# Kernel optimization log

Measured on AMD Instinct MI355X. Metric: run time of the kernel, lower is better.

Reference implementation:

```python
import jax, jax.numpy as jnp
import numpy as np

H, KV, D = 16, 4, 128
WIN = 512
EPS = 1e-6


def rms_norm(x, w):
    # x: [..., D]
    return x * jax.lax.rsqrt(jnp.mean(x * x, axis=-1, keepdims=True) + EPS) * w


def rotate_half(x):
    x1, x2 = jnp.split(x, 2, axis=-1)
    return jnp.concatenate([-x2, x1], axis=-1)


def setup_inputs() -> dict:
    key = jax.random.key(0)
    ks = jax.random.split(key, 8)
    B, L, hidden = 2, 2048, 2048
    x = jax.random.normal(ks[0], (B, L, hidden), jnp.float32)
    # realistic RoPE tables
    inv_freq = 1.0 / (10000.0 ** (np.arange(0, D, 2, dtype=np.float32) / D))
    t = np.arange(L, dtype=np.float32)
    freqs = np.outer(t, inv_freq)  # [L, D/2]
    emb = np.concatenate([freqs, freqs], axis=-1)  # [L, D]
    cos = jnp.asarray(np.cos(emb), jnp.float32)
    sin = jnp.asarray(np.sin(emb), jnp.float32)
    s = 0.02
    Wq = jax.random.normal(ks[1], (H * D, hidden), jnp.float32) * s
    Wk = jax.random.normal(ks[2], (KV * D, hidden), jnp.float32) * s
    Wv = jax.random.normal(ks[3], (KV * D, hidden), jnp.float32) * s
    Wo = jax.random.normal(ks[4], (hidden, H * D), jnp.float32) * s
    q_norm_w = jnp.ones((D,), jnp.float32)
    k_norm_w = jnp.ones((D,), jnp.float32)
    return {"x": x, "cos": cos, "sin": sin, "Wq": Wq, "Wk": Wk, "Wv": Wv,
            "Wo": Wo, "q_norm_w": q_norm_w, "k_norm_w": k_norm_w}


def reference(x, cos, sin, Wq, Wk, Wv, Wo, q_norm_w, k_norm_w):
    B, L, _ = x.shape
    # projections (torch Linear: y = x @ W.T)
    q = (x @ Wq.T).reshape(B, L, H, D)
    k = (x @ Wk.T).reshape(B, L, KV, D)
    v = (x @ Wv.T).reshape(B, L, KV, D)
    # QK RMSNorm, then [B, heads, L, D]
    q = jnp.transpose(rms_norm(q, q_norm_w), (0, 2, 1, 3))
    k = jnp.transpose(rms_norm(k, k_norm_w), (0, 2, 1, 3))
    v = jnp.transpose(v, (0, 2, 1, 3))
    # RoPE
    c = cos[None, None]  # [1,1,L,D]
    s = sin[None, None]
    q = q * c + rotate_half(q) * s
    k = k * c + rotate_half(k) * s
    # GQA repeat_interleave over head dim
    n_rep = H // KV
    k = jnp.repeat(k, n_rep, axis=1)
    v = jnp.repeat(v, n_rep, axis=1)
    # sliding-window additive bias [L, L]
    idx = jnp.arange(L)
    in_win = jnp.abs(idx[:, None] - idx[None, :]) <= WIN
    bias = jnp.where(in_win, 0.0, jnp.finfo(x.dtype).min).astype(x.dtype)
    # SDPA
    scale = 1.0 / jnp.sqrt(jnp.asarray(D, x.dtype))
    scores = jnp.einsum('bhqd,bhkd->bhqk', q, k) * scale + bias[None, None]
    attn = jax.nn.softmax(scores, axis=-1)
    out = jnp.einsum('bhqk,bhkd->bhqd', attn, v)  # [B,H,L,D]
    out = jnp.transpose(out, (0, 2, 1, 3)).reshape(B, L, H * D)
    return out @ Wo.T
```

## Files before the change

### kernel.cpp

```cpp
#include <hip/hip_runtime.h>
#include <hip/hip_bf16.h>


typedef unsigned short u16;
typedef unsigned int u32;
typedef __attribute__((ext_vector_type(8))) short bf16x8;
typedef __attribute__((ext_vector_type(4))) float f32x4;

#define AS1 __attribute__((address_space(1)))
#define AS3 __attribute__((address_space(3)))

__device__ __forceinline__ u16 f2b(float f) {
  union { float f; u32 u; } c; c.f = f;
  return (u16)((c.u + 0x8000u) >> 16);
}
__device__ __forceinline__ float b2f(u16 u) {
  union { u32 u; float f; } c; c.u = ((u32)u) << 16; return c.f;
}

__global__ __launch_bounds__(256) void cvt_all(const float* __restrict__ x,
                                               const float* __restrict__ wq,
                                               const float* __restrict__ wk,
                                               const float* __restrict__ wv,
                                               const float* __restrict__ wo,
                                               u16* __restrict__ xb,
                                               u16* __restrict__ wqkvb,
                                               u16* __restrict__ wob) {
  int blk = blockIdx.x;
  const float* s; u16* d; int off;
  if (blk < 8192)       { s = x;  d = xb;              off = blk * 1024; }
  else if (blk < 12288) { s = wq; d = wqkvb;           off = (blk - 8192) * 1024; }
  else if (blk < 13312) { s = wk; d = wqkvb + 4194304; off = (blk - 12288) * 1024; }
  else if (blk < 14336) { s = wv; d = wqkvb + 5242880; off = (blk - 13312) * 1024; }
  else                  { s = wo; d = wob;             off = (blk - 14336) * 1024; }
  int i = off + threadIdx.x * 4;
  float4 v = *(const float4*)(s + i);
  ushort4 o;
  o.x = f2b(v.x); o.y = f2b(v.y); o.z = f2b(v.z); o.w = f2b(v.w);
  *(ushort4*)(d + i) = o;
}

template<int F32OUT>
__global__ __launch_bounds__(256) void gemm_bt(const u16* __restrict__ A,
                                               const u16* __restrict__ Bm,
                                               void* __restrict__ C,
                                               int M, int N, int K) {
  __shared__ u16 As[128][64];
  __shared__ u16 Bs[128][64];
  const int tid  = threadIdx.x;
  const int w    = tid >> 6, lane = tid & 63, quad = lane >> 4, l16 = lane & 15;
  const int wm   = w >> 1, wn = w & 1;
  const int m0   = blockIdx.y * 128, n0 = blockIdx.x * 128;

  f32x4 zero = {0.f, 0.f, 0.f, 0.f};
  f32x4 acc[4][4];
#pragma unroll
  for (int i = 0; i < 4; i++)
#pragma unroll
    for (int j = 0; j < 4; j++) acc[i][j] = zero;

  const int srow = lane >> 3;
  const int swz8 = ((lane & 7) ^ (lane >> 3)) * 8;

  for (int k0 = 0; k0 < K; k0 += 64) {
#pragma unroll
    for (int p = 0; p < 4; ++p) {
      int row = p * 32 + w * 8 + srow;
      __builtin_amdgcn_global_load_lds(
          (const AS1 void*)(A + (size_t)(m0 + row) * K + k0 + swz8),
          (AS3 void*)((char*)&As[0][0] + p * 4096 + w * 1024), 16, 0, 0);
      __builtin_amdgcn_global_load_lds(
          (const AS1 void*)(Bm + (size_t)(n0 + row) * K + k0 + swz8),
          (AS3 void*)((char*)&Bs[0][0] + p * 4096 + w * 1024), 16, 0, 0);
    }
    __syncthreads();
#pragma unroll
    for (int kk = 0; kk < 64; kk += 32) {
      const int cs = ((kk >> 3) + quad) ^ (l16 & 7);
      bf16x8 af[4], bfr[4];
#pragma unroll
      for (int i = 0; i < 4; i++)
        af[i] = *(const bf16x8*)((const char*)&As[0][0] +
                                 (wm * 64 + i * 16 + l16) * 128 + cs * 16);
#pragma unroll
      for (int j = 0; j < 4; j++)
        bfr[j] = *(const bf16x8*)((const char*)&Bs[0][0] +
                                  (wn * 64 + j * 16 + l16) * 128 + cs * 16);
#pragma unroll
      for (int i = 0; i < 4; i++)
#pragma unroll
        for (int j = 0; j < 4; j++)
          acc[i][j] = __builtin_amdgcn_mfma_f32_16x16x32_bf16(af[i], bfr[j], acc[i][j], 0, 0, 0);
    }
    __syncthreads();
  }

#pragma unroll
  for (int i = 0; i < 4; i++) {
#pragma unroll
    for (int r = 0; r < 4; r++) {
      int gr = m0 + wm * 64 + i * 16 + quad * 4 + r;
#pragma unroll
      for (int j = 0; j < 4; j++) {
        int gc = n0 + wn * 64 + j * 16 + l16;
        if (F32OUT) ((float*)C)[(size_t)gr * N + gc] = acc[i][j][r];
        else        ((u16*)C)[(size_t)gr * N + gc]   = f2b(acc[i][j][r]);
      }
    }
  }
}

__global__ __launch_bounds__(256) void rmsrope(const u16* __restrict__ qkv,
                                               const float* __restrict__ cosT,
                                               const float* __restrict__ sinT,
                                               const float* __restrict__ qw,
                                               const float* __restrict__ kw,
                                               u16* __restrict__ qo,
                                               u16* __restrict__ ko) {
  int wid  = blockIdx.x * 4 + (threadIdx.x >> 6);
  int lane = threadIdx.x & 63;
  int r  = wid / 20;
  int hh = wid % 20;
  int b = r >> 11, l = r & 2047;
  int cb = hh < 16 ? hh * 128 : 2048 + (hh - 16) * 128;
  const u16* src = qkv + (size_t)r * 3072 + cb;
  float v0 = b2f(src[lane]);
  float v1 = b2f(src[lane + 64]);
  float ss = v0 * v0 + v1 * v1;
#pragma unroll
  for (int off = 1; off < 64; off <<= 1) ss += __shfl_xor(ss, off, 64);
  float inv = rsqrtf(ss * (1.0f / 128.0f) + 1e-6f);
  const float* wt = hh < 16 ? qw : kw;
  float n0 = v0 * inv * wt[lane];
  float n1 = v1 * inv * wt[lane + 64];
  float c0 = cosT[l * 128 + lane],      c1 = cosT[l * 128 + 64 + lane];
  float s0 = sinT[l * 128 + lane],      s1 = sinT[l * 128 + 64 + lane];
  float o0 = n0 * c0 - n1 * s0;
  float o1 = n1 * c1 + n0 * s1;
  const float qscale = 0.08838834764831845f * 1.4426950408889634f;
  u16* dst; size_t base;
  if (hh < 16) { dst = qo; base = ((size_t)(b * 16 + hh) * 2048 + l) * 128;
                 o0 *= qscale; o1 *= qscale; }
  else         { dst = ko; base = ((size_t)(b * 4 + (hh - 16)) * 2048 + l) * 128; }
  dst[base + lane]      = f2b(o0);
  dst[base + 64 + lane] = f2b(o1);
}

__global__ __launch_bounds__(256) void transpose_v(const u16* __restrict__ qkv,
                                                   u16* __restrict__ dst) {
  __shared__ u16 T[64][72];
  const int lt = blockIdx.x, dt = blockIdx.y, bh = blockIdx.z;
  const int b = bh >> 2, kv = bh & 3;
  const u16* s = qkv + ((size_t)(b * 2048 + lt * 64)) * 3072 + 2560 + kv * 128 + dt * 64;
  u16*       d = dst + (size_t)bh * 128 * 2048 + (size_t)dt * 64 * 2048 + lt * 64;
  const int t = threadIdx.x;
  const int row = t >> 3, c8 = (t & 7) * 8;
#pragma unroll
  for (int p = 0; p < 2; ++p)
    *(uint4*)&T[p * 32 + row][c8] = *(const uint4*)(s + (size_t)(p * 32 + row) * 3072 + c8);
  __syncthreads();
#pragma unroll
  for (int p = 0; p < 2; ++p) {
    int dr = p * 32 + row;
    u16 o[8];
#pragma unroll
    for (int j = 0; j < 8; ++j) o[j] = T[c8 + j][dr];
    *(uint4*)(d + (size_t)dr * 2048 + c8) = *(uint4*)o;
  }
}

__global__ __launch_bounds__(256) void flash_swa(const u16* __restrict__ Q,
                                                 const u16* __restrict__ Kg,
                                                 const u16* __restrict__ VTg,
                                                 u16* __restrict__ Og) {
  constexpr int L = 2048, D = 128;
  __shared__ u16 Ks[2][64][128];
  __shared__ u16 Vt[2][128][64];
  __shared__ u16 Ps[4][16][64];

  const int q0  = blockIdx.x * 64;
  const int h   = blockIdx.y;
  const int b   = blockIdx.z;
  const int tid = threadIdx.x;
  const int w = tid >> 6, lane = tid & 63, quad = lane >> 4, l16 = lane & 15;
  const int kvh = h >> 2;

  const u16* Qb  = Q   + (size_t)(b * 16 + h)  * L * D;
  const u16* Kb  = Kg  + (size_t)(b * 4 + kvh) * L * D;
  const u16* VTb = VTg + (size_t)(b * 4 + kvh) * D * L;

  bf16x8 qf[4];
  {
    int qr = q0 + w * 16 + l16;
#pragma unroll
    for (int ks = 0; ks < 4; ++ks)
      qf[ks] = *(const bf16x8*)(Qb + (size_t)qr * D + ks * 32 + quad * 8);
  }
  const int qi = q0 + w * 16 + l16;

  int kt0   = q0 > 512 ? q0 - 512 : 0;
  int ktend = q0 + 64 + 512; if (ktend > L) ktend = L;
  const int nt = (ktend - kt0) >> 6;

  const u16* srcK[4];
  const u16* srcV[4];
#pragma unroll
  for (int p = 0; p < 4; ++p) {
    int rk = w * 16 + p * 4 + (lane >> 4);
    int ck = ((lane & 15) ^ (rk & 7)) * 8;
    srcK[p] = Kb + (size_t)(kt0 + rk) * D + ck;
    int rv = w * 32 + p * 8 + (lane >> 3);
    int cv = ((lane & 7) ^ (rv & 7)) * 8;
    srcV[p] = VTb + (size_t)rv * L + kt0 + cv;
  }

#define STAGE(bb) do {                                                        \
    char* kdst = (char*)&Ks[bb][0][0] + w * 4096;                             \
    char* vdst = (char*)&Vt[bb][0][0] + w * 4096;                             \
    _Pragma("unroll")                                                         \
    for (int p = 0; p < 4; ++p) {                                             \
      __builtin_amdgcn_global_load_lds((const AS1 void*)srcK[p],              \
          (AS3 void*)(kdst + p * 1024), 16, 0, 0);                            \
      srcK[p] += 64 * D;                                                      \
    }                                                                         \
    _Pragma("unroll")                                                         \
    for (int p = 0; p < 4; ++p) {                                             \
      __builtin_amdgcn_global_load_lds((const AS1 void*)srcV[p],              \
          (AS3 void*)(vdst + p * 1024), 16, 0, 0);                            \
      srcV[p] += 64;                                                          \
    }                                                                         \
  } while (0)

  f32x4 zero = {0.f, 0.f, 0.f, 0.f};
  f32x4 o[8];
#pragma unroll
  for (int i = 0; i < 8; i++) o[i] = zero;
  float lrow = 0.f;

  STAGE(0);
  __syncthreads();
  int cur = 0;

  const int swz = (l16 & 7) << 4;

  for (int t = 0; t < nt; ++t) {
    const int kt = kt0 + t * 64;
    if (t + 1 < nt) STAGE(cur ^ 1);

    const char* kbase = (const char*)&Ks[cur][0][0];
    const char* vbase = (const char*)&Vt[cur][0][0];

    f32x4 s[4];
#pragma unroll
    for (int ct = 0; ct < 4; ct++) s[ct] = zero;
    __builtin_amdgcn_s_setprio(1);
#pragma unroll
    for (int ks = 0; ks < 4; ++ks) {
#pragma unroll
      for (int ct = 0; ct < 4; ++ct) {
        bf16x8 kf = *(const bf16x8*)(kbase + (ct * 16 + l16) * 256 +
                                     (((ks * 4 + quad) ^ (l16 & 7)) * 16));
        s[ct] = __builtin_amdgcn_mfma_f32_16x16x32_bf16(kf, qf[ks], s[ct], 0, 0, 0);
      }
    }
    __builtin_amdgcn_s_setprio(0);

    bool need_mask = (kt + 448 < q0) || (kt > q0 + 448);
    float psum = 0.f;
    char* psw = (char*)&Ps[w][l16][0];
#pragma unroll
    for (int ct = 0; ct < 4; ct++) {
      u16 ph[4];
#pragma unroll
      for (int r = 0; r < 4; r++) {
        float x = s[ct][r];
        if (need_mask) {
          int ki = kt + ct * 16 + quad * 4 + r;
          int dd = qi - ki; if (dd < 0) dd = -dd;
          if (dd > 512) x = -__builtin_inff();
        }
        float p = exp2f(x);
        psum += p;
        ph[r] = f2b(p);
      }
      uint2 pk;
      pk.x = (u32)ph[0] | ((u32)ph[1] << 16);
      pk.y = (u32)ph[2] | ((u32)ph[3] << 16);
      *(uint2*)(psw + ((ct * 32 + quad * 8) ^ swz)) = pk;
    }
    psum += __shfl_xor(psum, 16, 64);
    psum += __shfl_xor(psum, 32, 64);
    lrow += psum;

    bf16x8 pf[2];
#pragma unroll
    for (int ks2 = 0; ks2 < 2; ++ks2)
      pf[ks2] = *(const bf16x8*)(psw + ((ks2 * 64 + quad * 16) ^ swz));
    __builtin_amdgcn_s_setprio(1);
#pragma unroll
    for (int dt = 0; dt < 8; ++dt) {
#pragma unroll
      for (int ks2 = 0; ks2 < 2; ++ks2) {
        bf16x8 vf = *(const bf16x8*)(vbase + (dt * 16 + l16) * 128 +
                                     (((ks2 * 4 + quad) ^ (l16 & 7)) * 16));
        o[dt] = __builtin_amdgcn_mfma_f32_16x16x32_bf16(pf[ks2], vf, o[dt], 0, 0, 0);
      }
    }
    __builtin_amdgcn_s_setprio(0);

    __syncthreads();
    cur ^= 1;
  }
#undef STAGE

#pragma unroll
  for (int r = 0; r < 4; r++) {
    float lv  = __shfl(lrow, (lane & 48) + quad * 4 + r, 64);
    float inv = 1.0f / lv;
    int qr = q0 + w * 16 + quad * 4 + r;
    size_t base = ((size_t)(b * L + qr)) * 2048 + h * 128;
#pragma unroll
    for (int dt = 0; dt < 8; dt++)
      Og[base + dt * 16 + l16] = f2b(o[dt][r] * inv);
  }
}

extern "C" void kernel_launch(void* const* d_in, const int* in_sizes, int n_in,
                              void* d_out, int out_size, void* d_ws, size_t ws_size,
                              hipStream_t stream) {
  const float* x    = (const float*)d_in[0];
  const float* cosT = (const float*)d_in[1];
  const float* sinT = (const float*)d_in[2];
  const float* Wq   = (const float*)d_in[3];
  const float* Wk   = (const float*)d_in[4];
  const float* Wv   = (const float*)d_in[5];
  const float* Wo   = (const float*)d_in[6];
  const float* qw   = (const float*)d_in[7];
  const float* kw   = (const float*)d_in[8];

  char* ws = (char*)d_ws;
  u16* x_bf    = (u16*)(ws + 0);
  u16* wqkv_bf = (u16*)(ws + 16777216);
  u16* wo_bf   = (u16*)(ws + 29360128);
  u16* qkv_bf  = (u16*)(ws + 37748736);
  u16* q_bf    = (u16*)(ws + 62914560);
  u16* k_bf    = (u16*)(ws + 79691776);
  u16* vt_bf   = wqkv_bf;
  u16* attn_bf = x_bf;

  cvt_all<<<18432, 256, 0, stream>>>(x, Wq, Wk, Wv, Wo, x_bf, wqkv_bf, wo_bf);
  gemm_bt<0><<<dim3(24, 32), 256, 0, stream>>>(x_bf, wqkv_bf, qkv_bf, 4096, 3072, 2048);
  rmsrope<<<20480, 256, 0, stream>>>(qkv_bf, cosT, sinT, qw, kw, q_bf, k_bf);
  transpose_v<<<dim3(32, 2, 8), 256, 0, stream>>>(qkv_bf, vt_bf);
  flash_swa<<<dim3(32, 16, 2), 256, 0, stream>>>(q_bf, k_bf, vt_bf, attn_bf);
  gemm_bt<1><<<dim3(16, 32), 256, 0, stream>>>(attn_bf, wo_bf, d_out, 4096, 2048, 2048);
}
```

Baseline: 315.4 us.

## Share K/V tiles across all four GQA heads in one 512-thread flash block

Each attention block now handles all four query heads that share one KV head, with 8 waves each covering 32 query rows of one head, so every K/V tile staged into LDS is reused by four heads instead of being reloaded per head. The grid shrinks from 1024 to 256 blocks of 512 threads, and each wave keeps two 16-row Q fragments and two sets of accumulators. This cuts global K/V traffic, at the cost of higher register pressure, a larger P scratch buffer, and fewer blocks, which may leave CUs underused.

Measured after the change: 299.8 us. 1.05x faster.

```diff
diff --git a/kernel.cpp b/kernel.cpp
--- a/kernel.cpp
+++ b/kernel.cpp
@@ -169,73 +169,77 @@
   }
 }
 
-__global__ __launch_bounds__(256) void flash_swa(const u16* __restrict__ Q,
+__global__ __launch_bounds__(512) void flash_swa(const u16* __restrict__ Q,
                                                  const u16* __restrict__ Kg,
                                                  const u16* __restrict__ VTg,
                                                  u16* __restrict__ Og) {
   constexpr int L = 2048, D = 128;
   __shared__ u16 Ks[2][64][128];
   __shared__ u16 Vt[2][128][64];
-  __shared__ u16 Ps[4][16][64];
+  __shared__ u16 Ps[8][32][64];
 
   const int q0  = blockIdx.x * 64;
-  const int h   = blockIdx.y;
+  const int kvh = blockIdx.y;
   const int b   = blockIdx.z;
   const int tid = threadIdx.x;
   const int w = tid >> 6, lane = tid & 63, quad = lane >> 4, l16 = lane & 15;
-  const int kvh = h >> 2;
-
-  const u16* Qb  = Q   + (size_t)(b * 16 + h)  * L * D;
+  const int hd = kvh * 4 + (w >> 1);
+  const int qh = w & 1;
+
+  const u16* Qb  = Q   + (size_t)(b * 16 + hd)  * L * D;
   const u16* Kb  = Kg  + (size_t)(b * 4 + kvh) * L * D;
   const u16* VTb = VTg + (size_t)(b * 4 + kvh) * D * L;
 
-  bf16x8 qf[4];
-  {
-    int qr = q0 + w * 16 + l16;
+  bf16x8 qf[2][4];
+#pragma unroll
+  for (int qs = 0; qs < 2; ++qs) {
+    int qr = q0 + qh * 32 + qs * 16 + l16;
 #pragma unroll
     for (int ks = 0; ks < 4; ++ks)
-      qf[ks] = *(const bf16x8*)(Qb + (size_t)qr * D + ks * 32 + quad * 8);
-  }
-  const int qi = q0 + w * 16 + l16;
+      qf[qs][ks] = *(const bf16x8*)(Qb + (size_t)qr * D + ks * 32 + quad * 8);
+  }
+  const int qi0 = q0 + qh * 32 + l16;
 
   int kt0   = q0 > 512 ? q0 - 512 : 0;
   int ktend = q0 + 64 + 512; if (ktend > L) ktend = L;
   const int nt = (ktend - kt0) >> 6;
 
-  const u16* srcK[4];
-  const u16* srcV[4];
-#pragma unroll
-  for (int p = 0; p < 4; ++p) {
-    int rk = w * 16 + p * 4 + (lane >> 4);
+  const u16* srcK[2];
+  const u16* srcV[2];
+#pragma unroll
+  for (int j = 0; j < 2; ++j) {
+    int rk = w * 8 + j * 4 + quad;
     int ck = ((lane & 15) ^ (rk & 7)) * 8;
-    srcK[p] = Kb + (size_t)(kt0 + rk) * D + ck;
-    int rv = w * 32 + p * 8 + (lane >> 3);
-    int cv = ((lane & 7) ^ (rv & 7)) * 8;
-    srcV[p] = VTb + (size_t)rv * L + kt0 + cv;
+    srcK[j] = Kb + (size_t)(kt0 + rk) * D + ck;
+    int rv = w * 16 + j * 8 + (lane >> 3);
+    int cv = ((lane & 7) ^ ((lane >> 3) & 7)) * 8;
+    srcV[j] = VTb + (size_t)rv * L + kt0 + cv;
   }
 
 #define STAGE(bb) do {                                                        \
-    char* kdst = (char*)&Ks[bb][0][0] + w * 4096;                             \
-    char* vdst = (char*)&Vt[bb][0][0] + w * 4096;                             \
+    char* kdst = (char*)&Ks[bb][0][0] + w * 2048;                             \
+    char* vdst = (char*)&Vt[bb][0][0] + w * 2048;                             \
     _Pragma("unroll")                                                         \
-    for (int p = 0; p < 4; ++p) {                                             \
-      __builtin_amdgcn_global_load_lds((const AS1 void*)srcK[p],              \
-          (AS3 void*)(kdst + p * 1024), 16, 0, 0);                            \
-      srcK[p] += 64 * D;                                                      \
+    for (int j = 0; j < 2; ++j) {                                             \
+      __builtin_amdgcn_global_load_lds((const AS1 void*)srcK[j],              \
+          (AS3 void*)(kdst + j * 1024), 16, 0, 0);                            \
+      srcK[j] += 64 * D;                                                      \
     }                                                                         \
     _Pragma("unroll")                                                         \
-    for (int p = 0; p < 4; ++p) {                                             \
-      __builtin_amdgcn_global_load_lds((const AS1 void*)srcV[p],              \
-          (AS3 void*)(vdst + p * 1024), 16, 0, 0);                            \
-      srcV[p] += 64;                                                          \
+    for (int j = 0; j < 2; ++j) {                                             \
+      __builtin_amdgcn_global_load_lds((const AS1 void*)srcV[j],              \
+          (AS3 void*)(vdst + j * 1024), 16, 0, 0);                            \
+      srcV[j] += 64;                                                          \
     }                                                                         \
   } while (0)
 
   f32x4 zero = {0.f, 0.f, 0.f, 0.f};
-  f32x4 o[8];
-#pragma unroll
-  for (int i = 0; i < 8; i++) o[i] = zero;
-  float lrow = 0.f;
+  f32x4 o[2][8];
+#pragma unroll
+  for (int qs = 0; qs < 2; ++qs)
+#pragma unroll
+    for (int i = 0; i < 8; i++) o[qs][i] = zero;
+  float lrow[2] = {0.f, 0.f};
 
   STAGE(0);
   __syncthreads();
@@ -250,9 +254,11 @@
     const char* kbase = (const char*)&Ks[cur][0][0];
     const char* vbase = (const char*)&Vt[cur][0][0];
 
-    f32x4 s[4];
-#pragma unroll
-    for (int ct = 0; ct < 4; ct++) s[ct] = zero;
+    f32x4 s[2][4];
+#pragma unroll
+    for (int qs = 0; qs < 2; ++qs)
+#pragma unroll
+      for (int ct = 0; ct < 4; ct++) s[qs][ct] = zero;
     __builtin_amdgcn_s_setprio(1);
 #pragma unroll
     for (int ks = 0; ks < 4; ++ks) {
@@ -260,42 +266,50 @@
       for (int ct = 0; ct < 4; ++ct) {
         bf16x8 kf = *(const bf16x8*)(kbase + (ct * 16 + l16) * 256 +
                                      (((ks * 4 + quad) ^ (l16 & 7)) * 16));
-        s[ct] = __builtin_amdgcn_mfma_f32_16x16x32_bf16(kf, qf[ks], s[ct], 0, 0, 0);
+        s[0][ct] = __builtin_amdgcn_mfma_f32_16x16x32_bf16(kf, qf[0][ks], s[0][ct], 0, 0, 0);
+        s[1][ct] = __builtin_amdgcn_mfma_f32_16x16x32_bf16(kf, qf[1][ks], s[1][ct], 0, 0, 0);
       }
     }
     __builtin_amdgcn_s_setprio(0);
 
     bool need_mask = (kt + 448 < q0) || (kt > q0 + 448);
-    float psum = 0.f;
-    char* psw = (char*)&Ps[w][l16][0];
-#pragma unroll
-    for (int ct = 0; ct < 4; ct++) {
-      u16 ph[4];
-#pragma unroll
-      for (int r = 0; r < 4; r++) {
-        float x = s[ct][r];
-        if (need_mask) {
-          int ki = kt + ct * 16 + quad * 4 + r;
-          int dd = qi - ki; if (dd < 0) dd = -dd;
-          if (dd > 512) x = -__builtin_inff();
+#pragma unroll
+    for (int qs = 0; qs < 2; ++qs) {
+      float psum = 0.f;
+      char* psw = (char*)&Ps[w][qs * 16 + l16][0];
+#pragma unroll
+      for (int ct = 0; ct < 4; ct++) {
+        u16 ph[4];
+#pragma unroll
+        for (int r = 0; r < 4; r++) {
+          float x = s[qs][ct][r];
+          if (need_mask) {
+            int ki = kt + ct * 16 + quad * 4 + r;
+            int dd = (qi0 + qs * 16) - ki; if (dd < 0) dd = -dd;
+            if (dd > 512) x = -__builtin_inff();
+          }
+          float p = exp2f(x);
+          psum += p;
+          ph[r] = f2b(p);
         }
-        float p = exp2f(x);
-        psum += p;
-        ph[r] = f2b(p);
+        uint2 pk;
+        pk.x = (u32)ph[0] | ((u32)ph[1] << 16);
+        pk.y = (u32)ph[2] | ((u32)ph[3] << 16);
+        *(uint2*)(psw + ((ct * 32 + quad * 8) ^ swz)) = pk;
       }
-      uint2 pk;
-      pk.x = (u32)ph[0] | ((u32)ph[1] << 16);
-      pk.y = (u32)ph[2] | ((u32)ph[3] << 16);
-      *(uint2*)(psw + ((ct * 32 + quad * 8) ^ swz)) = pk;
-    }
-    psum += __shfl_xor(psum, 16, 64);
-    psum += __shfl_xor(psum, 32, 64);
-    lrow += psum;
-
-    bf16x8 pf[2];
-#pragma unroll
-    for (int ks2 = 0; ks2 < 2; ++ks2)
-      pf[ks2] = *(const bf16x8*)(psw + ((ks2 * 64 + quad * 16) ^ swz));
+      psum += __shfl_xor(psum, 16, 64);
+      psum += __shfl_xor(psum, 32, 64);
+      lrow[qs] += psum;
+    }
+
+    bf16x8 pf[2][2];
+#pragma unroll
+    for (int qs = 0; qs < 2; ++qs) {
+      const char* psw = (const char*)&Ps[w][qs * 16 + l16][0];
+#pragma unroll
+      for (int ks2 = 0; ks2 < 2; ++ks2)
+        pf[qs][ks2] = *(const bf16x8*)(psw + ((ks2 * 64 + quad * 16) ^ swz));
+    }
     __builtin_amdgcn_s_setprio(1);
 #pragma unroll
     for (int dt = 0; dt < 8; ++dt) {
@@ -303,7 +317,8 @@
       for (int ks2 = 0; ks2 < 2; ++ks2) {
         bf16x8 vf = *(const bf16x8*)(vbase + (dt * 16 + l16) * 128 +
                                      (((ks2 * 4 + quad) ^ (l16 & 7)) * 16));
-        o[dt] = __builtin_amdgcn_mfma_f32_16x16x32_bf16(pf[ks2], vf, o[dt], 0, 0, 0);
+        o[0][dt] = __builtin_amdgcn_mfma_f32_16x16x32_bf16(pf[0][ks2], vf, o[0][dt], 0, 0, 0);
+        o[1][dt] = __builtin_amdgcn_mfma_f32_16x16x32_bf16(pf[1][ks2], vf, o[1][dt], 0, 0, 0);
       }
     }
     __builtin_amdgcn_s_setprio(0);
@@ -314,14 +329,17 @@
 #undef STAGE
 
 #pragma unroll
-  for (int r = 0; r < 4; r++) {
-    float lv  = __shfl(lrow, (lane & 48) + quad * 4 + r, 64);
-    float inv = 1.0f / lv;
-    int qr = q0 + w * 16 + quad * 4 + r;
-    size_t base = ((size_t)(b * L + qr)) * 2048 + h * 128;
-#pragma unroll
-    for (int dt = 0; dt < 8; dt++)
-      Og[base + dt * 16 + l16] = f2b(o[dt][r] * inv);
+  for (int qs = 0; qs < 2; ++qs) {
+#pragma unroll
+    for (int r = 0; r < 4; r++) {
+      float lv  = __shfl(lrow[qs], (lane & 48) + quad * 4 + r, 64);
+      float inv = 1.0f / lv;
+      int qr = q0 + qh * 32 + qs * 16 + quad * 4 + r;
+      size_t base = ((size_t)(b * L + qr)) * 2048 + hd * 128;
+#pragma unroll
+      for (int dt = 0; dt < 8; dt++)
+        Og[base + dt * 16 + l16] = f2b(o[qs][dt][r] * inv);
+    }
   }
 }
 
@@ -352,6 +370,6 @@
   gemm_bt<0><<<dim3(24, 32), 256, 0, stream>>>(x_bf, wqkv_bf, qkv_bf, 4096, 3072, 2048);
   rmsrope<<<20480, 256, 0, stream>>>(qkv_bf, cosT, sinT, qw, kw, q_bf, k_bf);
   transpose_v<<<dim3(32, 2, 8), 256, 0, stream>>>(qkv_bf, vt_bf);
-  flash_swa<<<dim3(32, 16, 2), 256, 0, stream>>>(q_bf, k_bf, vt_bf, attn_bf);
+  flash_swa<<<dim3(32, 4, 2), 512, 0, stream>>>(q_bf, k_bf, vt_bf, attn_bf);
   gemm_bt<1><<<dim3(16, 32), 256, 0, stream>>>(attn_bf, wo_bf, d_out, 4096, 2048, 2048);
 }
```

## Share K/V tiles across the four GQA heads in one attention block

Applied to the files above, without the earlier changes.

Each flash attention block now holds 8 waves covering the 4 query heads that share one KV head, with 32 query rows per head. K and V tiles are staged into LDS once and reused by all four heads, instead of each head's block loading them separately. The aim is to cut global and L2 traffic for K/V by up to four times. The cost is a larger block size, a bigger LDS footprint for Ps, and partial-tile waste at the window edges because the 32-row query span no longer aligns to 64-key tiles.

After: 300.6 us. -4.7%, faster.

```diff
diff --git a/kernel.cpp b/kernel.cpp
--- a/kernel.cpp
+++ b/kernel.cpp
@@ -169,65 +169,65 @@
   }
 }
 
-__global__ __launch_bounds__(256) void flash_swa(const u16* __restrict__ Q,
-                                                 const u16* __restrict__ Kg,
-                                                 const u16* __restrict__ VTg,
-                                                 u16* __restrict__ Og) {
+__global__ __launch_bounds__(512, 4) void flash_swa(const u16* __restrict__ Q,
+                                                    const u16* __restrict__ Kg,
+                                                    const u16* __restrict__ VTg,
+                                                    u16* __restrict__ Og) {
   constexpr int L = 2048, D = 128;
   __shared__ u16 Ks[2][64][128];
   __shared__ u16 Vt[2][128][64];
-  __shared__ u16 Ps[4][16][64];
-
-  const int q0  = blockIdx.x * 64;
-  const int h   = blockIdx.y;
-  const int b   = blockIdx.z;
+  __shared__ u16 Ps[8][16][64];
+
+  const int flat = blockIdx.x;
+  const int kvh  = flat & 3;
+  const int b    = (flat >> 2) & 1;
+  const int q0   = (flat >> 3) * 32;
   const int tid = threadIdx.x;
   const int w = tid >> 6, lane = tid & 63, quad = lane >> 4, l16 = lane & 15;
-  const int kvh = h >> 2;
-
-  const u16* Qb  = Q   + (size_t)(b * 16 + h)  * L * D;
+  const int hd = kvh * 4 + (w >> 1);
+  const int qh = w & 1;
+
+  const u16* Qb  = Q   + (size_t)(b * 16 + hd)  * L * D;
   const u16* Kb  = Kg  + (size_t)(b * 4 + kvh) * L * D;
   const u16* VTb = VTg + (size_t)(b * 4 + kvh) * D * L;
 
   bf16x8 qf[4];
-  {
-    int qr = q0 + w * 16 + l16;
-#pragma unroll
-    for (int ks = 0; ks < 4; ++ks)
-      qf[ks] = *(const bf16x8*)(Qb + (size_t)qr * D + ks * 32 + quad * 8);
-  }
-  const int qi = q0 + w * 16 + l16;
-
-  int kt0   = q0 > 512 ? q0 - 512 : 0;
-  int ktend = q0 + 64 + 512; if (ktend > L) ktend = L;
+  const int qi = q0 + qh * 16 + l16;
+#pragma unroll
+  for (int ks = 0; ks < 4; ++ks)
+    qf[ks] = *(const bf16x8*)(Qb + (size_t)qi * D + ks * 32 + quad * 8);
+
+  int kt0   = q0 > 512 ? (q0 - 512) & ~63 : 0;
+  int ktend = q0 + 32 + 512; if (ktend > L) ktend = L;
+  ktend = (ktend + 63) & ~63;
   const int nt = (ktend - kt0) >> 6;
 
-  const u16* srcK[4];
-  const u16* srcV[4];
-#pragma unroll
-  for (int p = 0; p < 4; ++p) {
-    int rk = w * 16 + p * 4 + (lane >> 4);
+  const u16* srcK[2];
+  const u16* srcV[2];
+#pragma unroll
+  for (int j = 0; j < 2; ++j) {
+    int rk = w * 8 + j * 4 + quad;
     int ck = ((lane & 15) ^ (rk & 7)) * 8;
-    srcK[p] = Kb + (size_t)(kt0 + rk) * D + ck;
-    int rv = w * 32 + p * 8 + (lane >> 3);
-    int cv = ((lane & 7) ^ (rv & 7)) * 8;
-    srcV[p] = VTb + (size_t)rv * L + kt0 + cv;
+    srcK[j] = Kb + (size_t)(kt0 + rk) * D + ck;
+    int rv = w * 16 + j * 8 + (lane >> 3);
+    int cv = ((lane & 7) ^ ((lane >> 3) & 7)) * 8;
+    srcV[j] = VTb + (size_t)rv * L + kt0 + cv;
   }
 
 #define STAGE(bb) do {                                                        \
-    char* kdst = (char*)&Ks[bb][0][0] + w * 4096;                             \
-    char* vdst = (char*)&Vt[bb][0][0] + w * 4096;                             \
+    char* kdst = (char*)&Ks[bb][0][0] + w * 2048;                             \
+    char* vdst = (char*)&Vt[bb][0][0] + w * 2048;                             \
     _Pragma("unroll")                                                         \
-    for (int p = 0; p < 4; ++p) {                                             \
-      __builtin_amdgcn_global_load_lds((const AS1 void*)srcK[p],              \
-          (AS3 void*)(kdst + p * 1024), 16, 0, 0);                            \
-      srcK[p] += 64 * D;                                                      \
+    for (int j = 0; j < 2; ++j) {                                             \
+      __builtin_amdgcn_global_load_lds((const AS1 void*)srcK[j],              \
+          (AS3 void*)(kdst + j * 1024), 16, 0, 0);                            \
+      srcK[j] += 64 * D;                                                      \
     }                                                                         \
     _Pragma("unroll")                                                         \
-    for (int p = 0; p < 4; ++p) {                                             \
-      __builtin_amdgcn_global_load_lds((const AS1 void*)srcV[p],              \
-          (AS3 void*)(vdst + p * 1024), 16, 0, 0);                            \
-      srcV[p] += 64;                                                          \
+    for (int j = 0; j < 2; ++j) {                                             \
+      __builtin_amdgcn_global_load_lds((const AS1 void*)srcV[j],              \
+          (AS3 void*)(vdst + j * 1024), 16, 0, 0);                            \
+      srcV[j] += 64;                                                          \
     }                                                                         \
   } while (0)
 
@@ -265,7 +265,7 @@
     }
     __builtin_amdgcn_s_setprio(0);
 
-    bool need_mask = (kt + 448 < q0) || (kt > q0 + 448);
+    bool need_mask = (q0 - kt > 448) || (kt - q0 > 416);
     float psum = 0.f;
     char* psw = (char*)&Ps[w][l16][0];
 #pragma unroll
@@ -317,8 +317,8 @@
   for (int r = 0; r < 4; r++) {
     float lv  = __shfl(lrow, (lane & 48) + quad * 4 + r, 64);
     float inv = 1.0f / lv;
-    int qr = q0 + w * 16 + quad * 4 + r;
-    size_t base = ((size_t)(b * L + qr)) * 2048 + h * 128;
+    int qr = q0 + qh * 16 + quad * 4 + r;
+    size_t base = ((size_t)(b * L + qr)) * 2048 + hd * 128;
 #pragma unroll
     for (int dt = 0; dt < 8; dt++)
       Og[base + dt * 16 + l16] = f2b(o[dt][r] * inv);
@@ -352,6 +352,6 @@
   gemm_bt<0><<<dim3(24, 32), 256, 0, stream>>>(x_bf, wqkv_bf, qkv_bf, 4096, 3072, 2048);
   rmsrope<<<20480, 256, 0, stream>>>(qkv_bf, cosT, sinT, qw, kw, q_bf, k_bf);
   transpose_v<<<dim3(32, 2, 8), 256, 0, stream>>>(qkv_bf, vt_bf);
-  flash_swa<<<dim3(32, 16, 2), 256, 0, stream>>>(q_bf, k_bf, vt_bf, attn_bf);
+  flash_swa<<<dim3(512, 1, 1), 512, 0, stream>>>(q_bf, k_bf, vt_bf, attn_bf);
   gemm_bt<1><<<dim3(16, 32), 256, 0, stream>>>(attn_bf, wo_bf, d_out, 4096, 2048, 2048);
 }
```
